# Optimization experiments

Measured on AMD Instinct MI355X. Metric: run time of the kernel, lower is better.

Reference implementation:

```python
import jax, jax.numpy as jnp
import numpy as np

K_NEIGHBORS = 3


def setup_inputs() -> dict:
    key = jax.random.key(0)
    ks = jax.random.split(key, 16)
    B, N = 8, 2048
    s = 0.05
    p = {
        "x": jax.random.normal(ks[0], (B, N, 4), dtype=jnp.float32),
        "W1": jax.random.normal(ks[1], (4, 64), dtype=jnp.float32) * s,
        "b1": jnp.zeros((64,), jnp.float32),
        "W2": jax.random.normal(ks[2], (64, 64), dtype=jnp.float32) * s,
        "b2": jnp.zeros((64,), jnp.float32),
        "Wm": jax.random.normal(ks[3], (64, 64), dtype=jnp.float32) * s,
        "bm": jnp.zeros((64,), jnp.float32),
        "Wu1": jax.random.normal(ks[4], (128, 128), dtype=jnp.float32) * s,
        "bu1": jnp.zeros((128,), jnp.float32),
        "Wu2": jax.random.normal(ks[5], (128, 128), dtype=jnp.float32) * s,
        "bu2": jnp.zeros((128,), jnp.float32),
        "Wmean": jax.random.normal(ks[6], (128, 2), dtype=jnp.float32) * s,
        "bmean": jnp.zeros((2,), jnp.float32),
        "Wv": jax.random.normal(ks[7], (128, 1), dtype=jnp.float32) * s,
        "bv": jnp.zeros((1,), jnp.float32),
        "log_std": jnp.zeros((2,), jnp.float32),
    }
    return p


def reference(x, W1, b1, W2, b2, Wm, bm, Wu1, bu1, Wu2, bu2, Wmean, bmean, Wv, bv, log_std):
    # node MLP: [B,N,4] -> [B,N,64]
    h = jax.nn.relu(x @ W1 + b1)
    h = jax.nn.relu(h @ W2 + b2)
    # pairwise squared distances without materializing [B,N,N,64] diff:
    # ||a-b||^2 = ||a||^2 + ||b||^2 - 2 a.b  (same math as diff.pow(2).sum(-1))
    sq = jnp.sum(h * h, axis=-1)  # [B,N]
    gram = jnp.einsum("bnd,bmd->bnm", h, h)  # [B,N,N]
    dist = sq[:, :, None] + sq[:, None, :] - 2.0 * gram  # [B,N,N]
    # k smallest (ascending) = top_k of negated dist; drop self (index 0)
    _, idx = jax.lax.top_k(-dist, K_NEIGHBORS + 1)  # [B,N,K+1]
    knn_idx = idx[:, :, 1:]  # [B,N,K]
    # gather neighbor features: [B,N,K,64]
    neigh = jax.vmap(lambda hb, ib: hb[ib])(h, knn_idx)
    # msg MLP + mean over neighbors
    msgs = jax.nn.relu(neigh @ Wm + bm).mean(axis=2)  # [B,N,64]
    hc = jnp.concatenate([h, msgs], axis=-1)  # [B,N,128]
    u = jax.nn.relu(hc @ Wu1 + bu1)
    u = jax.nn.relu(u @ Wu2 + bu2)
    return (u @ Wmean + bmean, jnp.exp(log_std), u @ Wv + bv)
```

## Files before the change

kernel.cpp:

```cpp
#include <hip/hip_runtime.h>
#include <math.h>

#define NB 8
#define NN 2048

typedef short bf16x8 __attribute__((ext_vector_type(8)));
typedef float f32x4  __attribute__((ext_vector_type(4)));
typedef unsigned long long u64;

__device__ __forceinline__ f32x4 mfma16(uint4 a, uint4 b, f32x4 c) {
    return __builtin_amdgcn_mfma_f32_16x16x32_bf16(
        __builtin_bit_cast(bf16x8, a), __builtin_bit_cast(bf16x8, b), c, 0, 0, 0);
}

__device__ __forceinline__ float bf2f(unsigned short u) {
    unsigned int t = ((unsigned int)u) << 16;
    return __builtin_bit_cast(float, t);
}

__device__ __forceinline__ unsigned short f2bf_rne(float f) {
    unsigned int u = __builtin_bit_cast(unsigned int, f);
    return (unsigned short)((u + 0x7FFFu + ((u >> 16) & 1u)) >> 16);
}

__device__ __forceinline__ unsigned int rne_pair(unsigned int a, unsigned int b, unsigned int c) {
    float lo = bf2f((unsigned short)(a & 0xFFFF)) + bf2f((unsigned short)(b & 0xFFFF)) + bf2f((unsigned short)(c & 0xFFFF));
    float hi = bf2f((unsigned short)(a >> 16)) + bf2f((unsigned short)(b >> 16)) + bf2f((unsigned short)(c >> 16));
    return (unsigned int)f2bf_rne(lo) | ((unsigned int)f2bf_rne(hi) << 16);
}
__device__ __forceinline__ uint4 rne_merge(uint4 a, uint4 b, uint4 c) {
    return make_uint4(rne_pair(a.x, b.x, c.x), rne_pair(a.y, b.y, c.y),
                      rne_pair(a.z, b.z, c.z), rne_pair(a.w, b.w, c.w));
}

__device__ __forceinline__ u64 packdj(float d, int j) {
    unsigned int u = __builtin_bit_cast(unsigned int, d);
    unsigned int key = u ^ ((unsigned int)(((int)u) >> 31) | 0x80000000u);
    return ((u64)key << 32) | (unsigned int)j;
}

#define INS4(vv, ii, d, j) {                                      \
    bool c0 = (d < vv.x) || (d == vv.x && j < ii.x);              \
    bool c1 = (d < vv.y) || (d == vv.y && j < ii.y);              \
    bool c2 = (d < vv.z) || (d == vv.z && j < ii.z);              \
    bool c3 = (d < vv.w) || (d == vv.w && j < ii.w);              \
    vv.w = c3 ? (c2 ? vv.z : d) : vv.w; ii.w = c3 ? (c2 ? ii.z : j) : ii.w; \
    vv.z = c2 ? (c1 ? vv.y : d) : vv.z; ii.z = c2 ? (c1 ? ii.y : j) : ii.z; \
    vv.y = c1 ? (c0 ? vv.x : d) : vv.y; ii.y = c1 ? (c0 ? ii.x : j) : ii.y; \
    vv.x = c0 ? d : vv.x;               ii.x = c0 ? j : ii.x; }

#define INS4S(vv, ii, d, j) {                                     \
    bool c0 = (d < vv.x); bool c1 = (d < vv.y);                   \
    bool c2 = (d < vv.z); bool c3 = (d < vv.w);                   \
    vv.w = c3 ? (c2 ? vv.z : d) : vv.w; ii.w = c3 ? (c2 ? ii.z : j) : ii.w; \
    vv.z = c2 ? (c1 ? vv.y : d) : vv.z; ii.z = c2 ? (c1 ? ii.y : j) : ii.z; \
    vv.y = c1 ? (c0 ? vv.x : d) : vv.y; ii.y = c1 ? (c0 ? ii.x : j) : ii.y; \
    vv.x = c0 ? d : vv.x;               ii.x = c0 ? j : ii.x; }

#define INSQ(a0, a1, a2, a3, p) {                                 \
    bool c0 = (p) < a0; bool c1 = (p) < a1;                       \
    bool c2 = (p) < a2; bool c3 = (p) < a3;                       \
    a3 = c3 ? (c2 ? a2 : (p)) : a3;                               \
    a2 = c2 ? (c1 ? a1 : (p)) : a2;                               \
    a1 = c1 ? (c0 ? a0 : (p)) : a1;                               \
    a0 = c0 ? (p) : a0; }

__global__ __launch_bounds__(256) void k_wprep(
    const float* __restrict__ Wm, const float* __restrict__ Wu1, const float* __restrict__ Wu2,
    uint4* __restrict__ wfrag)
{
    int q = blockIdx.x * 256 + threadIdx.x;
    int ln = q & 63;
    int fr = ln & 15, qd = ln >> 4;
    unsigned int p[4];
    if (q < 512) {
        int fi2 = q >> 6;
        int fg = fi2 >> 1, hf = fi2 & 1;
        #pragma unroll
        for (int e2 = 0; e2 < 4; e2++) {
            unsigned int lo = f2bf_rne(Wm[(hf * 32 + qd * 8 + e2 * 2 + 0) * 64 + fg * 16 + fr]);
            unsigned int hi = f2bf_rne(Wm[(hf * 32 + qd * 8 + e2 * 2 + 1) * 64 + fg * 16 + fr]);
            p[e2] = lo | (hi << 16);
        }
    } else {
        int qq = q - 512;
        const float* W = (qq < 2048) ? Wu1 : Wu2;
        int q2 = qq & 2047;
        int fi2 = q2 >> 6;
        int fg = fi2 >> 2, kq = fi2 & 3;
        #pragma unroll
        for (int e2 = 0; e2 < 4; e2++) {
            unsigned int lo = f2bf_rne(W[(kq * 32 + qd * 8 + e2 * 2 + 0) * 128 + fg * 16 + fr]);
            unsigned int hi = f2bf_rne(W[(kq * 32 + qd * 8 + e2 * 2 + 1) * 128 + fg * 16 + fr]);
            p[e2] = lo | (hi << 16);
        }
    }
    wfrag[q] = make_uint4(p[0], p[1], p[2], p[3]);
}

__global__ __launch_bounds__(256) void k_embed(
    const float* __restrict__ x, const float* __restrict__ W1, const float* __restrict__ b1,
    const float* __restrict__ W2, const float* __restrict__ b2,
    uint4* __restrict__ HsF, float* __restrict__ sqv)
{
    __shared__ float w2s[4096];
    __shared__ float h1s[4][4][64];
    __shared__ unsigned short sh[3 * 16 * 72];
    int tid = threadIdx.x;
    for (int q = tid; q < 4096; q += 256) w2s[q] = W2[q];
    int wave = tid >> 6, lane = tid & 63;
    int nbase = blockIdx.x * 16 + wave * 4;
    float w10 = W1[lane], w11 = W1[64 + lane], w12 = W1[128 + lane], w13 = W1[192 + lane];
    float b1l = b1[lane];
    #pragma unroll
    for (int v = 0; v < 4; v++) {
        float4 xv = reinterpret_cast<const float4*>(x)[nbase + v];
        h1s[wave][v][lane] = fmaxf(b1l + xv.x * w10 + xv.y * w11 + xv.z * w12 + xv.w * w13, 0.f);
    }
    __syncthreads();
    float b2l = b2[lane];
    float a0 = b2l, a1 = b2l, a2 = b2l, a3 = b2l;
    for (int k = 0; k < 64; k++) {
        float w = w2s[k * 64 + lane];
        a0 += h1s[wave][0][k] * w; a1 += h1s[wave][1][k] * w;
        a2 += h1s[wave][2][k] * w; a3 += h1s[wave][3][k] * w;
    }
    float hvs[4] = {fmaxf(a0, 0.f), fmaxf(a1, 0.f), fmaxf(a2, 0.f), fmaxf(a3, 0.f)};
    #pragma unroll
    for (int v = 0; v < 4; v++) {
        float hval = hvs[v];
        long node = nbase + v;
        int row = wave * 4 + v;
        unsigned int u0 = __builtin_bit_cast(unsigned int, hval);
        unsigned short s0 = (unsigned short)(u0 >> 16);
        float f0 = __builtin_bit_cast(float, u0 & 0xFFFF0000u);
        float r1 = hval - f0;
        unsigned int u1 = __builtin_bit_cast(unsigned int, r1);
        unsigned short s1 = (unsigned short)(u1 >> 16);
        float f1 = __builtin_bit_cast(float, u1 & 0xFFFF0000u);
        float r2 = r1 - f1;
        unsigned short s2 = (unsigned short)(__builtin_bit_cast(unsigned int, r2) >> 16);
        sh[(0 * 16 + row) * 72 + lane] = s0;
        sh[(1 * 16 + row) * 72 + lane] = s1;
        sh[(2 * 16 + row) * 72 + lane] = s2;
        float s = hval * hval;
        #pragma unroll
        for (int m = 1; m < 64; m <<= 1) s += __shfl_xor(s, m, 64);
        if (lane == 0) sqv[node] = s;
    }
    __syncthreads();
    for (int q = tid; q < 384; q += 256) {
        int f = q >> 6, ln = q & 63;
        int s = f >> 1, hf = f & 1;
        int row = ln & 15, eb = hf * 32 + (ln >> 4) * 8;
        const unsigned short* sp = &sh[(s * 16 + row) * 72 + eb];
        unsigned int p0 = (unsigned int)sp[0] | ((unsigned int)sp[1] << 16);
        unsigned int p1 = (unsigned int)sp[2] | ((unsigned int)sp[3] << 16);
        unsigned int p2 = (unsigned int)sp[4] | ((unsigned int)sp[5] << 16);
        unsigned int p3 = (unsigned int)sp[6] | ((unsigned int)sp[7] << 16);
        HsF[((long)blockIdx.x * 6 + f) * 64 + ln] = make_uint4(p0, p1, p2, p3);
    }
}

__global__ __launch_bounds__(256, 3) void k_knn(
    const uint4* __restrict__ HsF, const float* __restrict__ sqv,
    u64* __restrict__ pk)
{
    __shared__ float smv[4][1056];
    __shared__ int   smi[4][1056];

    int tid = threadIdx.x;
    int wave = tid >> 6, lane = tid & 63;
    int l15 = lane & 15, quad = lane >> 4;

    int bx = blockIdx.x;
    int js = bx & 3;
    int gquad = (bx >> 2) & 31;
    int b = bx >> 7;
    int gwb = gquad * 4 + wave;
    long g = (long)b * 128 + gwb;
    const float* sqb = sqv + ((long)b << 11);

    uint4 A[6];
    #pragma unroll
    for (int f = 0; f < 6; f++)
        A[f] = HsF[(g * 6 + f) * 64 + lane];

    float4 val[4]; int4 idx[4];
    #pragma unroll
    for (int r = 0; r < 4; r++) {
        val[r] = make_float4(3.4e38f, 3.4e38f, 3.4e38f, 3.4e38f);
        idx[r] = make_int4(0x7fffffff, 0x7fffffff, 0x7fffffff, 0x7fffffff);
    }

#define LOADB(B, SJ, G) {                                                     \
    long fb = ((long)b * 128 + (G)) * 6;                                      \
    _Pragma("unroll")                                                         \
    for (int f = 0; f < 6; f++)                                               \
        B[f] = HsF[(fb + f) * 64 + lane];                                     \
    SJ = sqb[(G) * 16 + l15]; }

#define COMPUTE(B, SJ, G) {                                                   \
    int j = (G) * 16 + l15;                                                   \
    f32x4 acc = {0.f, 0.f, 0.f, 0.f};                                         \
    _Pragma("unroll")                                                         \
    for (int hf = 0; hf < 2; hf++) {                                          \
        acc = mfma16(A[hf],     B[hf],     acc);                              \
        acc = mfma16(A[hf],     B[2 + hf], acc);                              \
        acc = mfma16(A[2 + hf], B[hf],     acc);                              \
        acc = mfma16(A[2 + hf], B[2 + hf], acc);                              \
        acc = mfma16(A[hf],     B[4 + hf], acc);                              \
        acc = mfma16(A[4 + hf], B[hf],     acc);                              \
    }                                                                         \
    _Pragma("unroll")                                                         \
    for (int r = 0; r < 4; r++) {                                             \
        float d = fmaf(-2.f, acc[r], SJ);                                     \
        INS4S(val[r], idx[r], d, j);                                          \
    } }

    int jg0 = js * 32;
    uint4 B0[6], B1[6];
    float sj0, sj1;
    LOADB(B0, sj0, jg0);
    #pragma unroll 1
    for (int t = 0; t < 16; t++) {
        int ga = jg0 + t * 2;
        int gbn = ga + 1;
        int gc = jg0 + ((t * 2 + 2) & 31);
        LOADB(B1, sj1, gbn);
        COMPUTE(B0, sj0, ga);
        LOADB(B0, sj0, gc);
        COMPUTE(B1, sj1, gbn);
    }

    float* mv = smv[wave]; int* mi = smi[wave];
    #pragma unroll
    for (int r = 0; r < 4; r++) {
        int base = (quad * 4 + r) * 65 + l15 * 4;
        mv[base + 0] = val[r].x; mv[base + 1] = val[r].y;
        mv[base + 2] = val[r].z; mv[base + 3] = val[r].w;
        mi[base + 0] = idx[r].x; mi[base + 1] = idx[r].y;
        mi[base + 2] = idx[r].z; mi[base + 3] = idx[r].w;
    }
    __syncthreads();
    float4 fv = make_float4(3.4e38f, 3.4e38f, 3.4e38f, 3.4e38f);
    int4   fi = make_int4(0x7fffffff, 0x7fffffff, 0x7fffffff, 0x7fffffff);
    #pragma unroll
    for (int tt = 0; tt < 4; tt++) {
        int base = l15 * 65 + (quad * 4 + tt) * 4;
        #pragma unroll
        for (int k = 0; k < 4; k++) {
            float d = mv[base + k];
            int j = mi[base + k];
            INS4(fv, fi, d, j);
        }
    }
    #pragma unroll
    for (int m = 16; m <= 32; m <<= 1) {
        float ov0 = __shfl_xor(fv.x, m, 64), ov1 = __shfl_xor(fv.y, m, 64);
        float ov2 = __shfl_xor(fv.z, m, 64), ov3 = __shfl_xor(fv.w, m, 64);
        int   oi0 = __shfl_xor(fi.x, m, 64), oi1 = __shfl_xor(fi.y, m, 64);
        int   oi2 = __shfl_xor(fi.z, m, 64), oi3 = __shfl_xor(fi.w, m, 64);
        INS4(fv, fi, ov0, oi0); INS4(fv, fi, ov1, oi1);
        INS4(fv, fi, ov2, oi2); INS4(fv, fi, ov3, oi3);
    }
    if (quad == 0) {
        long node = ((long)b << 11) + gwb * 16 + l15;
        u64* dst = pk + node * 16 + js * 4;
        reinterpret_cast<ulonglong2*>(dst)[0] =
            make_ulonglong2(packdj(fv.x, fi.x), packdj(fv.y, fi.y));
        reinterpret_cast<ulonglong2*>(dst)[1] =
            make_ulonglong2(packdj(fv.z, fi.z), packdj(fv.w, fi.w));
    }
}

__global__ __launch_bounds__(256) void k_head(
    const uint4* __restrict__ HsF, const u64* __restrict__ pk, const uint4* __restrict__ wfrag,
    const float* __restrict__ bm, const float* __restrict__ bu1, const float* __restrict__ bu2,
    const float* __restrict__ Wmean, const float* __restrict__ bmean,
    const float* __restrict__ Wv, const float* __restrict__ bv,
    const float* __restrict__ log_std,
    float* __restrict__ out_mean, float* __restrict__ out_std, float* __restrict__ out_val)
{
    __shared__ __align__(16) unsigned short hcT[4][16 * 136];

    int tid = threadIdx.x;
    int wave = tid >> 6, lane = tid & 63;
    int l15 = lane & 15, quad = lane >> 4;
    long g = blockIdx.x * 4 + wave;
    int b = (int)(g >> 7);

    int nb[3];
    {
        const u64* src = pk + ((long)g * 16 + l15) * 16 + quad * 4;
        ulonglong2 a01 = reinterpret_cast<const ulonglong2*>(src)[0];
        ulonglong2 a23 = reinterpret_cast<const ulonglong2*>(src)[1];
        u64 m0 = a01.x, m1 = a01.y, m2 = a23.x, m3 = a23.y;
        #pragma unroll
        for (int m = 16; m <= 32; m <<= 1) {
            u64 p0 = __shfl_xor(m0, m, 64), p1 = __shfl_xor(m1, m, 64);
            u64 p2 = __shfl_xor(m2, m, 64), p3 = __shfl_xor(m3, m, 64);
            INSQ(m0, m1, m2, m3, p0); INSQ(m0, m1, m2, m3, p1);
            INSQ(m0, m1, m2, m3, p2); INSQ(m0, m1, m2, m3, p3);
        }
        nb[0] = (int)(unsigned int)m1;
        nb[1] = (int)(unsigned int)m2;
        nb[2] = (int)(unsigned int)m3;
    }

    uint4 hA[2];
    #pragma unroll
    for (int hf = 0; hf < 2; hf++)
        hA[hf] = rne_merge(HsF[(g * 6 + hf) * 64 + lane],
                           HsF[(g * 6 + 2 + hf) * 64 + lane],
                           HsF[(g * 6 + 4 + hf) * 64 + lane]);
    uint4 nA[3][2];
    #pragma unroll
    for (int e = 0; e < 3; e++) {
        int jn = nb[e];
        long gj = (long)b * 128 + (jn >> 4);
        int ln2 = quad * 16 + (jn & 15);
        #pragma unroll
        for (int hf = 0; hf < 2; hf++)
            nA[e][hf] = rne_merge(HsF[(gj * 6 + hf) * 64 + ln2],
                                  HsF[(gj * 6 + 2 + hf) * 64 + ln2],
                                  HsF[(gj * 6 + 4 + hf) * 64 + ln2]);
    }
    #pragma unroll
    for (int hf = 0; hf < 2; hf++)
        *reinterpret_cast<uint4*>(&hcT[wave][l15 * 136 + hf * 32 + quad * 8]) = hA[hf];
    __syncthreads();

    {
        uint4 wm_r[4][2];
        #pragma unroll
        for (int fg = 0; fg < 4; fg++)
            #pragma unroll
            for (int hf = 0; hf < 2; hf++)
                wm_r[fg][hf] = wfrag[(fg * 2 + hf) * 64 + lane];
        float bmv[4];
        #pragma unroll
        for (int fg = 0; fg < 4; fg++) bmv[fg] = bm[fg * 16 + l15];
        f32x4 msum[4];
        #pragma unroll
        for (int fg = 0; fg < 4; fg++) msum[fg] = (f32x4){0.f, 0.f, 0.f, 0.f};
        #pragma unroll
        for (int e = 0; e < 3; e++)
            #pragma unroll
            for (int fg = 0; fg < 4; fg++) {
                f32x4 c = {0.f, 0.f, 0.f, 0.f};
                c = mfma16(nA[e][0], wm_r[fg][0], c);
                c = mfma16(nA[e][1], wm_r[fg][1], c);
                #pragma unroll
                for (int r = 0; r < 4; r++) msum[fg][r] += fmaxf(c[r] + bmv[fg], 0.f);
            }
        #pragma unroll
        for (int fg = 0; fg < 4; fg++)
            #pragma unroll
            for (int r = 0; r < 4; r++)
                hcT[wave][(quad * 4 + r) * 136 + 64 + fg * 16 + l15] = f2bf_rne(msum[fg][r] * (1.f / 3.f));
    }
    __syncthreads();

    {
        uint4 a1[4];
        #pragma unroll
        for (int kq = 0; kq < 4; kq++)
            a1[kq] = *reinterpret_cast<const uint4*>(&hcT[wave][l15 * 136 + kq * 32 + quad * 8]);
        unsigned short u1s[8][4];
        #pragma unroll
        for (int fg = 0; fg < 8; fg++) {
            float bv1 = bu1[fg * 16 + l15];
            f32x4 c = {0.f, 0.f, 0.f, 0.f};
            #pragma unroll
            for (int kq = 0; kq < 4; kq++)
                c = mfma16(a1[kq], wfrag[512 + (fg * 4 + kq) * 64 + lane], c);
            #pragma unroll
            for (int r = 0; r < 4; r++) u1s[fg][r] = f2bf_rne(fmaxf(c[r] + bv1, 0.f));
        }
        __syncthreads();
        #pragma unroll
        for (int fg = 0; fg < 8; fg++)
            #pragma unroll
            for (int r = 0; r < 4; r++)
                hcT[wave][(quad * 4 + r) * 136 + fg * 16 + l15] = u1s[fg][r];
    }
    __syncthreads();

    float u2v[8][4];
    {
        uint4 a2[4];
        #pragma unroll
        for (int kq = 0; kq < 4; kq++)
            a2[kq] = *reinterpret_cast<const uint4*>(&hcT[wave][l15 * 136 + kq * 32 + quad * 8]);
        #pragma unroll
        for (int fg = 0; fg < 8; fg++) {
            float bv2 = bu2[fg * 16 + l15];
            f32x4 c = {0.f, 0.f, 0.f, 0.f};
            #pragma unroll
            for (int kq = 0; kq < 4; kq++)
                c = mfma16(a2[kq], wfrag[2560 + (fg * 4 + kq) * 64 + lane], c);
            #pragma unroll
            for (int r = 0; r < 4; r++) u2v[fg][r] = fmaxf(c[r] + bv2, 0.f);
        }
    }

    {
        float wm0[8], wm1[8], wvv[8];
        #pragma unroll
        for (int fg = 0; fg < 8; fg++) {
            int f = fg * 16 + l15;
            wm0[fg] = Wmean[f * 2 + 0];
            wm1[fg] = Wmean[f * 2 + 1];
            wvv[fg] = Wv[f];
        }
        float bm0 = bmean[0], bm1 = bmean[1], bv0 = bv[0];
        #pragma unroll
        for (int r = 0; r < 4; r++) {
            float p0 = 0.f, p1 = 0.f, p2 = 0.f;
            #pragma unroll
            for (int fg = 0; fg < 8; fg++) {
                p0 = fmaf(u2v[fg][r], wm0[fg], p0);
                p1 = fmaf(u2v[fg][r], wm1[fg], p1);
                p2 = fmaf(u2v[fg][r], wvv[fg], p2);
            }
            #pragma unroll
            for (int m = 1; m < 16; m <<= 1) {
                p0 += __shfl_xor(p0, m, 64);
                p1 += __shfl_xor(p1, m, 64);
                p2 += __shfl_xor(p2, m, 64);
            }
            if (l15 == 0) {
                int node = (int)g * 16 + quad * 4 + r;
                out_mean[node * 2 + 0] = p0 + bm0;
                out_mean[node * 2 + 1] = p1 + bm1;
                out_val[node] = p2 + bv0;
            }
        }
    }
    if (blockIdx.x == 0 && tid < 2) out_std[tid] = expf(log_std[tid]);
}

extern "C" void kernel_launch(void* const* d_in, const int* in_sizes, int n_in,
                              void* d_out, int out_size, void* d_ws, size_t ws_size,
                              hipStream_t stream) {
    const float* x     = (const float*)d_in[0];
    const float* W1    = (const float*)d_in[1];
    const float* b1    = (const float*)d_in[2];
    const float* W2    = (const float*)d_in[3];
    const float* b2    = (const float*)d_in[4];
    const float* Wm    = (const float*)d_in[5];
    const float* bm    = (const float*)d_in[6];
    const float* Wu1   = (const float*)d_in[7];
    const float* bu1   = (const float*)d_in[8];
    const float* Wu2   = (const float*)d_in[9];
    const float* bu2   = (const float*)d_in[10];
    const float* Wmean = (const float*)d_in[11];
    const float* bmean = (const float*)d_in[12];
    const float* Wv    = (const float*)d_in[13];
    const float* bv    = (const float*)d_in[14];
    const float* lstd  = (const float*)d_in[15];

    float* out = (float*)d_out;
    float* out_mean = out;
    float* out_std  = out + 32768;
    float* out_val  = out + 32770;

    uint4* HsF   = (uint4*)d_ws;
    float* sqv   = (float*)(HsF + (long)1024 * 6 * 64);
    uint4* wfrag = (uint4*)(sqv + 16384);
    u64*   pk    = (u64*)(wfrag + 4608);

    k_wprep<<<18, 256, 0, stream>>>(Wm, Wu1, Wu2, wfrag);
    k_embed<<<1024, 256, 0, stream>>>(x, W1, b1, W2, b2, HsF, sqv);
    k_knn<<<1024, 256, 0, stream>>>(HsF, sqv, pk);
    k_head<<<256, 256, 0, stream>>>(HsF, pk, wfrag, bm, bu1, bu2,
                                    Wmean, bmean, Wv, bv, lstd,
                                    out_mean, out_std, out_val);
}
```

Before: 196.7 us.

## Share neighbor tiles across waves via double-buffered LDS staging in kNN kernel

In the kNN kernel, every wave used to load all six B fragments for each neighbor tile from global memory on its own. Now the four waves cooperatively load the tile once, each wave taking three fragments, into a double-buffered LDS stage that is unioned with the reduction scratch space. This cuts redundant global/L2 traffic by a factor of four, at the cost of a block-wide barrier per iteration and LDS reads feeding the MFMAs. The embed kernel's packed output store is also changed to a single aligned 16-byte LDS read.

Measured after the change: 232.6 us. 1.18x slower.

```diff
diff --git a/kernel.cpp b/kernel.cpp
--- a/kernel.cpp
+++ b/kernel.cpp
@@ -105,7 +105,7 @@
 {
     __shared__ float w2s[4096];
     __shared__ float h1s[4][4][64];
-    __shared__ unsigned short sh[3 * 16 * 72];
+    __shared__ __align__(16) unsigned short sh[3 * 16 * 72];
     int tid = threadIdx.x;
     for (int q = tid; q < 4096; q += 256) w2s[q] = W2[q];
     int wave = tid >> 6, lane = tid & 63;
@@ -153,12 +153,8 @@
         int f = q >> 6, ln = q & 63;
         int s = f >> 1, hf = f & 1;
         int row = ln & 15, eb = hf * 32 + (ln >> 4) * 8;
-        const unsigned short* sp = &sh[(s * 16 + row) * 72 + eb];
-        unsigned int p0 = (unsigned int)sp[0] | ((unsigned int)sp[1] << 16);
-        unsigned int p1 = (unsigned int)sp[2] | ((unsigned int)sp[3] << 16);
-        unsigned int p2 = (unsigned int)sp[4] | ((unsigned int)sp[5] << 16);
-        unsigned int p3 = (unsigned int)sp[6] | ((unsigned int)sp[7] << 16);
-        HsF[((long)blockIdx.x * 6 + f) * 64 + ln] = make_uint4(p0, p1, p2, p3);
+        HsF[((long)blockIdx.x * 6 + f) * 64 + ln] =
+            *reinterpret_cast<const uint4*>(&sh[(s * 16 + row) * 72 + eb]);
     }
 }
 
@@ -166,8 +162,10 @@
     const uint4* __restrict__ HsF, const float* __restrict__ sqv,
     u64* __restrict__ pk)
 {
-    __shared__ float smv[4][1056];
-    __shared__ int   smi[4][1056];
+    __shared__ union SMem {
+        uint4 stage[2][2][6][64];
+        struct { float mv[4][1056]; int mi[4][1056]; } m;
+    } sm;
 
     int tid = threadIdx.x;
     int wave = tid >> 6, lane = tid & 63;
@@ -193,47 +191,65 @@
         idx[r] = make_int4(0x7fffffff, 0x7fffffff, 0x7fffffff, 0x7fffffff);
     }
 
-#define LOADB(B, SJ, G) {                                                     \
-    long fb = ((long)b * 128 + (G)) * 6;                                      \
+    int jg0 = js * 32;
+    uint4 N[3];
+    int fi0 = wave * 3;
+
+#define ISSUE(T) {                                                            \
     _Pragma("unroll")                                                         \
-    for (int f = 0; f < 6; f++)                                               \
-        B[f] = HsF[(fb + f) * 64 + lane];                                     \
-    SJ = sqb[(G) * 16 + l15]; }
-
-#define COMPUTE(B, SJ, G) {                                                   \
-    int j = (G) * 16 + l15;                                                   \
-    f32x4 acc = {0.f, 0.f, 0.f, 0.f};                                         \
+    for (int k = 0; k < 3; k++) {                                             \
+        int fi = fi0 + k; int gi2 = fi / 6, f = fi % 6;                       \
+        int G = jg0 + (T) * 2 + gi2;                                          \
+        N[k] = HsF[(((long)b * 128 + G) * 6 + f) * 64 + lane];                \
+    } }
+
+#define WRITE(BUF) {                                                          \
     _Pragma("unroll")                                                         \
-    for (int hf = 0; hf < 2; hf++) {                                          \
-        acc = mfma16(A[hf],     B[hf],     acc);                              \
-        acc = mfma16(A[hf],     B[2 + hf], acc);                              \
-        acc = mfma16(A[2 + hf], B[hf],     acc);                              \
-        acc = mfma16(A[2 + hf], B[2 + hf], acc);                              \
-        acc = mfma16(A[hf],     B[4 + hf], acc);                              \
-        acc = mfma16(A[4 + hf], B[hf],     acc);                              \
-    }                                                                         \
+    for (int k = 0; k < 3; k++) {                                             \
+        int fi = fi0 + k; int gi2 = fi / 6, f = fi % 6;                       \
+        sm.stage[BUF][gi2][f][lane] = N[k];                                   \
+    } }
+
+#define COMPUTE(BUF, T) {                                                     \
     _Pragma("unroll")                                                         \
-    for (int r = 0; r < 4; r++) {                                             \
-        float d = fmaf(-2.f, acc[r], SJ);                                     \
-        INS4S(val[r], idx[r], d, j);                                          \
+    for (int gi2 = 0; gi2 < 2; gi2++) {                                       \
+        int G = jg0 + (T) * 2 + gi2;                                          \
+        float sj = sqb[G * 16 + l15];                                         \
+        uint4 B[6];                                                           \
+        _Pragma("unroll")                                                     \
+        for (int f = 0; f < 6; f++)                                           \
+            B[f] = sm.stage[BUF][gi2][f][lane];                               \
+        f32x4 acc = {0.f, 0.f, 0.f, 0.f};                                     \
+        _Pragma("unroll")                                                     \
+        for (int hf = 0; hf < 2; hf++) {                                      \
+            acc = mfma16(A[hf],     B[hf],     acc);                          \
+            acc = mfma16(A[hf],     B[2 + hf], acc);                          \
+            acc = mfma16(A[2 + hf], B[hf],     acc);                          \
+            acc = mfma16(A[2 + hf], B[2 + hf], acc);                          \
+            acc = mfma16(A[hf],     B[4 + hf], acc);                          \
+            acc = mfma16(A[4 + hf], B[hf],     acc);                          \
+        }                                                                     \
+        int j = G * 16 + l15;                                                 \
+        _Pragma("unroll")                                                     \
+        for (int r = 0; r < 4; r++) {                                         \
+            float d = fmaf(-2.f, acc[r], sj);                                 \
+            INS4S(val[r], idx[r], d, j);                                      \
+        }                                                                     \
     } }
 
-    int jg0 = js * 32;
-    uint4 B0[6], B1[6];
-    float sj0, sj1;
-    LOADB(B0, sj0, jg0);
+    ISSUE(0)
+    WRITE(0)
+    ISSUE(1)
     #pragma unroll 1
     for (int t = 0; t < 16; t++) {
-        int ga = jg0 + t * 2;
-        int gbn = ga + 1;
-        int gc = jg0 + ((t * 2 + 2) & 31);
-        LOADB(B1, sj1, gbn);
-        COMPUTE(B0, sj0, ga);
-        LOADB(B0, sj0, gc);
-        COMPUTE(B1, sj1, gbn);
-    }
-
-    float* mv = smv[wave]; int* mi = smi[wave];
+        __syncthreads();
+        if (t < 15) WRITE((t + 1) & 1);
+        if (t < 14) ISSUE(t + 2);
+        COMPUTE(t & 1, t)
+    }
+
+    __syncthreads();
+    float* mv = sm.m.mv[wave]; int* mi = sm.m.mi[wave];
     #pragma unroll
     for (int r = 0; r < 4; r++) {
         int base = (quad * 4 + r) * 65 + l15 * 4;
```
